# Kernel tuning notes

Hardware: AMD Instinct MI355X
Metric: run time of the kernel (lower is better)

## Reference

```python
import jax, jax.numpy as jnp
import numpy as np

B, T, C = 32, 4096, 256


def setup_inputs() -> dict:
    key = jax.random.key(0)
    ks = jax.random.split(key, 10)
    s = lambda *sh: 0.05
    return {
        "gru_output": jax.random.normal(ks[0], (B, T, C), jnp.float32),
        "intensity_curves": jax.random.uniform(ks[1], (B, T), jnp.float32),
        "W1": jax.random.normal(ks[2], (C, 128), jnp.float32) * 0.05,
        "b1": jnp.zeros((128,), jnp.float32),
        "W2": jax.random.normal(ks[3], (128, 64), jnp.float32) * 0.05,
        "b2": jnp.zeros((64,), jnp.float32),
        "W3": jax.random.normal(ks[4], (64, 4), jnp.float32) * 0.05,
        "b3": jnp.zeros((4,), jnp.float32),
        "conv_w": jax.random.normal(ks[5], (1, C, 3), jnp.float32) * 0.05,  # OIH
        "conv_b": jnp.zeros((1,), jnp.float32),
    }


def reference(gru_output, intensity_curves, W1, b1, W2, b2, W3, b3, conv_w, conv_b):
    Bb, Tt, Cc = gru_output.shape
    # per-timestep phase classifier MLP + softmax -> (B,T,4)
    h = jax.nn.relu(gru_output @ W1 + b1)
    h = jax.nn.relu(h @ W2 + b2)
    phase_probs = jax.nn.softmax(h @ W3 + b3, axis=-1)
    # transition scores: Conv1d(C->1,k=3,pad=1) + sigmoid -> (B,T)
    x = jnp.transpose(gru_output, (0, 2, 1))  # (B,C,T)
    ts = jax.lax.conv_general_dilated(x, conv_w, (1,), 'SAME',
                                      dimension_numbers=('NCH', 'OIH', 'NCH'))
    transition_scores = jax.nn.sigmoid(ts[:, 0, :] + conv_b[0])  # (B,T)
    # run-length segments: new segment when dominant phase changes or transition>0.7
    dom = jnp.argmax(phase_probs, axis=-1)  # (B,T) int
    change = (dom[:, 1:] != dom[:, :-1]) | (transition_scores[:, 1:] > 0.7)
    change = jnp.concatenate([jnp.zeros((Bb, 1), bool), change], axis=1)
    seg = jnp.cumsum(change.astype(jnp.int32), axis=1)  # (B,T) segment id per step
    gseg = (seg + jnp.arange(Bb, dtype=jnp.int32)[:, None] * Tt).reshape(-1)
    nseg = Bb * Tt
    cnt = jax.ops.segment_sum(jnp.ones((nseg,), jnp.float32)[: gseg.shape[0]] * 0 + 1.0,
                              gseg, num_segments=nseg)
    sum_int = jax.ops.segment_sum(intensity_curves.reshape(-1), gseg, num_segments=nseg)
    conf_t = jnp.take_along_axis(phase_probs, dom[..., None], axis=2)[..., 0]  # (B,T)
    sum_conf = jax.ops.segment_sum(conf_t.reshape(-1), gseg, num_segments=nseg)
    denom = jnp.maximum(cnt, 1.0)
    mean_int = (sum_int / denom)[gseg].reshape(Bb, Tt)   # segment-mean intensity per step
    mean_conf = (sum_conf / denom)[gseg].reshape(Bb, Tt)  # segment-mean confidence per step
    return phase_probs, transition_scores, seg, mean_int, mean_conf
```

## Files before the change

### kernel.cpp

```cpp
#include <hip/hip_runtime.h>

#define B_ 32
#define T_ 4096
#define C_ 256
#define R_ (B_*T_)
#define H1_ 128
#define H2_ 64

#define TB 32

#define PROBS_OFF 0
#define TS_OFF  (R_*4)
#define SEG_OFF (TS_OFF + R_)
#define MI_OFF  (SEG_OFF + R_)
#define MC_OFF  (MI_OFF + R_)

#define XS_OFF  0
#define XS_P    260
#define W1S_OFF 8320
#define H1S_OFF 8320
#define H1S_P   132
#define H2S_OFF 0
#define H2S_P   68
#define W3S_OFF 2176
#define W3S_P   68
#define SMEMF   12544

__device__ __forceinline__ void fma4(float4& a, float s, const float4& b) {
  a.x = fmaf(s, b.x, a.x); a.y = fmaf(s, b.y, a.y);
  a.z = fmaf(s, b.z, a.z); a.w = fmaf(s, b.w, a.w);
}

__global__ __launch_bounds__(256, 4) void mlp_conv_kernel(
    const float* __restrict__ X, const float* __restrict__ W1, const float* __restrict__ b1,
    const float* __restrict__ W2, const float* __restrict__ b2,
    const float* __restrict__ W3, const float* __restrict__ b3,
    const float* __restrict__ CW, const float* __restrict__ CB,
    float* __restrict__ out)
{
  __shared__ float sm[SMEMF];
  const int tid  = threadIdx.x;
  const int row0 = blockIdx.x * TB;

  float4 st0 = *(const float4*)&W1[0 * 1024 + tid * 4];
  float4 st1 = *(const float4*)&W1[1 * 1024 + tid * 4];
  float4 st2 = *(const float4*)&W1[2 * 1024 + tid * 4];
  float4 st3 = *(const float4*)&W1[3 * 1024 + tid * 4];

  #pragma unroll
  for (int i2 = 0; i2 < 8; ++i2) {
    int g = tid + 256 * i2;
    int r = g >> 6, m = g & 63;
    float4 v = *(const float4*)&X[(size_t)(row0 + r) * C_ + m * 4];
    *(float4*)&sm[XS_OFF + r * XS_P + m * 4] = v;
  }
  __syncthreads();

  {
    const int l = tid & 63, w = tid >> 6;
    const int rowi = w * 8 + (l & 7);
    const int p = l >> 3;
    const int grow = row0 + rowi;
    const int tb = grow & (T_ - 1);
    float s = 0.f;
    #pragma unroll
    for (int cc = 0; cc < 8; ++cc) {
      const int c = p * 32 + cc * 4;
      float4 x0 = *(const float4*)&sm[XS_OFF + rowi * XS_P + c];
      float4 xm, xp;
      if (tb == 0)             xm = make_float4(0.f, 0.f, 0.f, 0.f);
      else if (rowi >= 1)      xm = *(const float4*)&sm[XS_OFF + (rowi - 1) * XS_P + c];
      else                     xm = *(const float4*)&X[(size_t)(grow - 1) * C_ + c];
      if (tb == T_ - 1)        xp = make_float4(0.f, 0.f, 0.f, 0.f);
      else if (rowi + 1 < TB)  xp = *(const float4*)&sm[XS_OFF + (rowi + 1) * XS_P + c];
      else                     xp = *(const float4*)&X[(size_t)(grow + 1) * C_ + c];
      float4 wa = *(const float4*)&CW[c * 3 + 0];
      float4 wb = *(const float4*)&CW[c * 3 + 4];
      float4 wc = *(const float4*)&CW[c * 3 + 8];
      s += xm.x * wa.x + x0.x * wa.y + xp.x * wa.z;
      s += xm.y * wa.w + x0.y * wb.x + xp.y * wb.y;
      s += xm.z * wb.z + x0.z * wb.w + xp.z * wc.x;
      s += xm.w * wc.y + x0.w * wc.z + xp.w * wc.w;
    }
    s += __shfl_xor(s, 8);
    s += __shfl_xor(s, 16);
    s += __shfl_xor(s, 32);
    if (p == 0) out[TS_OFF + grow] = 1.f / (1.f + expf(-(s + CB[0])));
  }

  const int rt = tid >> 5, ct = tid & 31;
  const int rb = rt * 4;
  float4 acc0 = make_float4(0.f, 0.f, 0.f, 0.f);
  float4 acc1 = acc0, acc2 = acc0, acc3 = acc0;
  for (int kc = 0; kc < 8; ++kc) {
    *(float4*)&sm[W1S_OFF + 0 * 1024 + tid * 4] = st0;
    *(float4*)&sm[W1S_OFF + 1 * 1024 + tid * 4] = st1;
    *(float4*)&sm[W1S_OFF + 2 * 1024 + tid * 4] = st2;
    *(float4*)&sm[W1S_OFF + 3 * 1024 + tid * 4] = st3;
    __syncthreads();
    if (kc + 1 < 8) {
      const float* wp = W1 + (size_t)(kc + 1) * 4096;
      st0 = *(const float4*)&wp[0 * 1024 + tid * 4];
      st1 = *(const float4*)&wp[1 * 1024 + tid * 4];
      st2 = *(const float4*)&wp[2 * 1024 + tid * 4];
      st3 = *(const float4*)&wp[3 * 1024 + tid * 4];
    }
    #pragma unroll
    for (int k4 = 0; k4 < 8; ++k4) {
      const int kb = kc * 32 + k4 * 4;
      float4 a0 = *(const float4*)&sm[XS_OFF + (rb + 0) * XS_P + kb];
      float4 a1 = *(const float4*)&sm[XS_OFF + (rb + 1) * XS_P + kb];
      float4 a2 = *(const float4*)&sm[XS_OFF + (rb + 2) * XS_P + kb];
      float4 a3 = *(const float4*)&sm[XS_OFF + (rb + 3) * XS_P + kb];
      float4 q0 = *(const float4*)&sm[W1S_OFF + (k4 * 4 + 0) * H1_ + ct * 4];
      float4 q1 = *(const float4*)&sm[W1S_OFF + (k4 * 4 + 1) * H1_ + ct * 4];
      float4 q2 = *(const float4*)&sm[W1S_OFF + (k4 * 4 + 2) * H1_ + ct * 4];
      float4 q3 = *(const float4*)&sm[W1S_OFF + (k4 * 4 + 3) * H1_ + ct * 4];
      fma4(acc0, a0.x, q0); fma4(acc0, a0.y, q1); fma4(acc0, a0.z, q2); fma4(acc0, a0.w, q3);
      fma4(acc1, a1.x, q0); fma4(acc1, a1.y, q1); fma4(acc1, a1.z, q2); fma4(acc1, a1.w, q3);
      fma4(acc2, a2.x, q0); fma4(acc2, a2.y, q1); fma4(acc2, a2.z, q2); fma4(acc2, a2.w, q3);
      fma4(acc3, a3.x, q0); fma4(acc3, a3.y, q1); fma4(acc3, a3.z, q2); fma4(acc3, a3.w, q3);
    }
    __syncthreads();
  }

  {
    float4 bb = *(const float4*)&b1[ct * 4];
    float4 h;
    h = acc0; h.x = fmaxf(h.x + bb.x, 0.f); h.y = fmaxf(h.y + bb.y, 0.f);
              h.z = fmaxf(h.z + bb.z, 0.f); h.w = fmaxf(h.w + bb.w, 0.f);
    *(float4*)&sm[H1S_OFF + (rb + 0) * H1S_P + ct * 4] = h;
    h = acc1; h.x = fmaxf(h.x + bb.x, 0.f); h.y = fmaxf(h.y + bb.y, 0.f);
              h.z = fmaxf(h.z + bb.z, 0.f); h.w = fmaxf(h.w + bb.w, 0.f);
    *(float4*)&sm[H1S_OFF + (rb + 1) * H1S_P + ct * 4] = h;
    h = acc2; h.x = fmaxf(h.x + bb.x, 0.f); h.y = fmaxf(h.y + bb.y, 0.f);
              h.z = fmaxf(h.z + bb.z, 0.f); h.w = fmaxf(h.w + bb.w, 0.f);
    *(float4*)&sm[H1S_OFF + (rb + 2) * H1S_P + ct * 4] = h;
    h = acc3; h.x = fmaxf(h.x + bb.x, 0.f); h.y = fmaxf(h.y + bb.y, 0.f);
              h.z = fmaxf(h.z + bb.z, 0.f); h.w = fmaxf(h.w + bb.w, 0.f);
    *(float4*)&sm[H1S_OFF + (rb + 3) * H1S_P + ct * 4] = h;
  }
  __syncthreads();

  {
    const int rt2 = tid >> 4, ct2 = tid & 15;
    const float* w2p = W2 + ct2 * 4;
    float4 Wc0 = *(const float4*)&w2p[0 * H2_];
    float4 Wc1 = *(const float4*)&w2p[1 * H2_];
    float4 Wc2 = *(const float4*)&w2p[2 * H2_];
    float4 Wc3 = *(const float4*)&w2p[3 * H2_];
    float4 c0 = make_float4(0.f, 0.f, 0.f, 0.f), c1 = c0;
    #pragma unroll
    for (int k4 = 0; k4 < 32; ++k4) {
      const int rn = (k4 < 31) ? (k4 + 1) * 4 : k4 * 4;
      float4 Wn0 = *(const float4*)&w2p[(rn + 0) * H2_];
      float4 Wn1 = *(const float4*)&w2p[(rn + 1) * H2_];
      float4 Wn2 = *(const float4*)&w2p[(rn + 2) * H2_];
      float4 Wn3 = *(const float4*)&w2p[(rn + 3) * H2_];
      float4 a0 = *(const float4*)&sm[H1S_OFF + (rt2 * 2 + 0) * H1S_P + k4 * 4];
      float4 a1 = *(const float4*)&sm[H1S_OFF + (rt2 * 2 + 1) * H1S_P + k4 * 4];
      fma4(c0, a0.x, Wc0); fma4(c0, a0.y, Wc1); fma4(c0, a0.z, Wc2); fma4(c0, a0.w, Wc3);
      fma4(c1, a1.x, Wc0); fma4(c1, a1.y, Wc1); fma4(c1, a1.z, Wc2); fma4(c1, a1.w, Wc3);
      Wc0 = Wn0; Wc1 = Wn1; Wc2 = Wn2; Wc3 = Wn3;
    }
    float4 bb = *(const float4*)&b2[ct2 * 4];
    c0.x = fmaxf(c0.x + bb.x, 0.f); c0.y = fmaxf(c0.y + bb.y, 0.f);
    c0.z = fmaxf(c0.z + bb.z, 0.f); c0.w = fmaxf(c0.w + bb.w, 0.f);
    c1.x = fmaxf(c1.x + bb.x, 0.f); c1.y = fmaxf(c1.y + bb.y, 0.f);
    c1.z = fmaxf(c1.z + bb.z, 0.f); c1.w = fmaxf(c1.w + bb.w, 0.f);
    *(float4*)&sm[H2S_OFF + (rt2 * 2 + 0) * H2S_P + ct2 * 4] = c0;
    *(float4*)&sm[H2S_OFF + (rt2 * 2 + 1) * H2S_P + ct2 * 4] = c1;
  }
  {
    int k = tid >> 2, j = tid & 3;
    sm[W3S_OFF + j * W3S_P + k] = W3[tid];
  }
  __syncthreads();

  if (tid < 128) {
    const int row = tid >> 2, j = tid & 3;
    float4 ps = make_float4(0.f, 0.f, 0.f, 0.f);
    #pragma unroll
    for (int k4 = 0; k4 < 16; ++k4) {
      float4 a = *(const float4*)&sm[H2S_OFF + row * H2S_P + k4 * 4];
      float4 w = *(const float4*)&sm[W3S_OFF + j * W3S_P + k4 * 4];
      ps.x = fmaf(a.x, w.x, ps.x);
      ps.y = fmaf(a.y, w.y, ps.y);
      ps.z = fmaf(a.z, w.z, ps.z);
      ps.w = fmaf(a.w, w.w, ps.w);
    }
    float l = ((ps.x + ps.y) + (ps.z + ps.w)) + b3[j];
    float n1v = __shfl_xor(l, 1);
    float n2v = __shfl_xor(l, 2);
    float n3v = __shfl_xor(l, 3);
    float L0 = (j == 0) ? l : (j == 1) ? n1v : (j == 2) ? n2v : n3v;
    float L1 = (j == 1) ? l : (j == 0) ? n1v : (j == 2) ? n3v : n2v;
    float L2 = (j == 2) ? l : (j == 0) ? n2v : (j == 1) ? n3v : n1v;
    float L3 = (j == 3) ? l : (j == 0) ? n3v : (j == 1) ? n2v : n1v;
    float mx = fmaxf(fmaxf(L0, L1), fmaxf(L2, L3));
    float e0 = expf(L0 - mx), e1 = expf(L1 - mx), e2 = expf(L2 - mx), e3 = expf(L3 - mx);
    float inv = 1.f / ((e0 + e1) + (e2 + e3));
    float p0 = e0 * inv, p1 = e1 * inv, p2 = e2 * inv, p3 = e3 * inv;
    const int grow = row0 + row;
    float pown = (j == 0) ? p0 : (j == 1) ? p1 : (j == 2) ? p2 : p3;
    out[PROBS_OFF + (size_t)grow * 4 + j] = pown;
    if (j == 0) {
      int dom = 0; float pm = p0;
      if (p1 > pm) { pm = p1; dom = 1; }
      if (p2 > pm) { pm = p2; dom = 2; }
      if (p3 > pm) { pm = p3; dom = 3; }
      out[MI_OFF + grow] = (float)dom;
      out[MC_OFF + grow] = pm;
    }
  }
}

__global__ __launch_bounds__(1024, 1) void seg_kernel(
    const float* __restrict__ inten, float* __restrict__ out)
{
  __shared__ float scnt[T_], ssi[T_], ssc[T_];
  __shared__ int wtot[16], wexcl[16];
  const int tid = threadIdx.x;
  const int lane = tid & 63, wid = tid >> 6;
  const size_t base = (size_t)blockIdx.x * T_;
  const float* tsS = out + TS_OFF;
  float* segO = out + SEG_OFF;
  float* miO  = out + MI_OFF;
  float* mcO  = out + MC_OFF;
  const int t4 = tid * 4;

  float4 dv = *(const float4*)&miO[base + t4];
  float4 tv = *(const float4*)&tsS[base + t4];
  float4 iv = *(const float4*)&inten[base + t4];
  float4 cv = *(const float4*)&mcO[base + t4];
  float pd = (tid == 0) ? 0.f : miO[base + t4 - 1];

  for (int i = tid; i < T_; i += 1024) { scnt[i] = 0.f; ssi[i] = 0.f; ssc[i] = 0.f; }

  int c0 = (t4 == 0) ? 0 : (((dv.x != pd)   || (tv.x > 0.7f)) ? 1 : 0);
  int c1 = ((dv.y != dv.x) || (tv.y > 0.7f)) ? 1 : 0;
  int c2 = ((dv.z != dv.y) || (tv.z > 0.7f)) ? 1 : 0;
  int c3 = ((dv.w != dv.z) || (tv.w > 0.7f)) ? 1 : 0;
  int l0 = c0, l1 = c0 + c1, l2 = l1 + c2, l3 = l2 + c3;
  const int tsum = l3;

  int v = tsum;
  #pragma unroll
  for (int d = 1; d < 64; d <<= 1) {
    int o = __shfl_up(v, (unsigned)d);
    if (lane >= d) v += o;
  }
  if (lane == 63) wtot[wid] = v;
  __syncthreads();
  if (tid < 16) {
    int x = wtot[tid];
    int xx = x;
    #pragma unroll
    for (int d = 1; d < 16; d <<= 1) {
      int o = __shfl_up(xx, (unsigned)d);
      if (tid >= d) xx += o;
    }
    wexcl[tid] = xx - x;
  }
  __syncthreads();
  const int texcl = wexcl[wid] + (v - tsum);
  const int s0 = texcl + l0, s1 = texcl + l1, s2 = texcl + l2, s3 = texcl + l3;

  {
    int cur = s0; float aI = iv.x, aC = cv.x, aN = 1.f;
    if (s1 == cur) { aI += iv.y; aC += cv.y; aN += 1.f; }
    else { atomicAdd(&ssi[cur], aI); atomicAdd(&ssc[cur], aC); atomicAdd(&scnt[cur], aN);
           cur = s1; aI = iv.y; aC = cv.y; aN = 1.f; }
    if (s2 == cur) { aI += iv.z; aC += cv.z; aN += 1.f; }
    else { atomicAdd(&ssi[cur], aI); atomicAdd(&ssc[cur], aC); atomicAdd(&scnt[cur], aN);
           cur = s2; aI = iv.z; aC = cv.z; aN = 1.f; }
    if (s3 == cur) { aI += iv.w; aC += cv.w; aN += 1.f; }
    else { atomicAdd(&ssi[cur], aI); atomicAdd(&ssc[cur], aC); atomicAdd(&scnt[cur], aN);
           cur = s3; aI = iv.w; aC = cv.w; aN = 1.f; }
    atomicAdd(&ssi[cur], aI); atomicAdd(&ssc[cur], aC); atomicAdd(&scnt[cur], aN);
  }
  __syncthreads();

  float n0 = scnt[s0], n1 = scnt[s1], n2 = scnt[s2], n3 = scnt[s3];
  float4 m4, q4, g4;
  m4.x = ssi[s0] / n0; m4.y = ssi[s1] / n1; m4.z = ssi[s2] / n2; m4.w = ssi[s3] / n3;
  q4.x = ssc[s0] / n0; q4.y = ssc[s1] / n1; q4.z = ssc[s2] / n2; q4.w = ssc[s3] / n3;
  g4.x = (float)s0; g4.y = (float)s1; g4.z = (float)s2; g4.w = (float)s3;
  *(float4*)&segO[base + t4] = g4;
  *(float4*)&miO[base + t4]  = m4;
  *(float4*)&mcO[base + t4]  = q4;
}

extern "C" void kernel_launch(void* const* d_in, const int* in_sizes, int n_in,
                              void* d_out, int out_size, void* d_ws, size_t ws_size,
                              hipStream_t stream) {
  (void)in_sizes; (void)n_in; (void)out_size; (void)d_ws; (void)ws_size;
  const float* X   = (const float*)d_in[0];
  const float* INT = (const float*)d_in[1];
  const float* W1  = (const float*)d_in[2];
  const float* B1  = (const float*)d_in[3];
  const float* W2  = (const float*)d_in[4];
  const float* B2  = (const float*)d_in[5];
  const float* W3  = (const float*)d_in[6];
  const float* B3  = (const float*)d_in[7];
  const float* CW  = (const float*)d_in[8];
  const float* CB  = (const float*)d_in[9];
  float* out = (float*)d_out;

  hipLaunchKernelGGL(mlp_conv_kernel, dim3(R_ / TB), dim3(256), 0, stream,
                     X, W1, B1, W2, B2, W3, B3, CW, CB, out);
  hipLaunchKernelGGL(seg_kernel, dim3(B_), dim3(1024), 0, stream, INT, out);
}
```

Measured before the change: 205.8 us.

## Stage W2 in shared memory, prefetch it during layer 1, fuse layer 3 via shuffles

W2 is now prefetched into registers during the last layer-1 iteration and stored to shared memory, so layer 2 reads weights from LDS instead of per-thread global loads. Layer 3 and the softmax are computed directly from the layer-2 register results with a cross-lane shuffle reduction, which removes the H2 shared-memory staging and one barrier. Probabilities are written as one float4 per row. This raises register pressure from the extra prefetched W2/W3 values, which may affect occupancy.

```diff
diff --git a/kernel.cpp b/kernel.cpp
--- a/kernel.cpp
+++ b/kernel.cpp
@@ -20,10 +20,7 @@
 #define W1S_OFF 8320
 #define H1S_OFF 8320
 #define H1S_P   132
-#define H2S_OFF 0
-#define H2S_P   68
-#define W3S_OFF 2176
-#define W3S_P   68
+#define W2S_OFF 0
 #define SMEMF   12544
 
 __device__ __forceinline__ void fma4(float4& a, float s, const float4& b) {
@@ -104,6 +101,11 @@
       st1 = *(const float4*)&wp[1 * 1024 + tid * 4];
       st2 = *(const float4*)&wp[2 * 1024 + tid * 4];
       st3 = *(const float4*)&wp[3 * 1024 + tid * 4];
+    } else {
+      st0 = ((const float4*)W2)[tid +   0];
+      st1 = ((const float4*)W2)[tid + 256];
+      st2 = ((const float4*)W2)[tid + 512];
+      st3 = ((const float4*)W2)[tid + 768];
     }
     #pragma unroll
     for (int k4 = 0; k4 < 8; ++k4) {
@@ -124,6 +126,16 @@
     __syncthreads();
   }
 
+  const int ct2 = tid & 15;
+  float4 t4a = ((const float4*)W2)[tid + 1024];
+  float4 t4b = ((const float4*)W2)[tid + 1280];
+  float4 t4c = ((const float4*)W2)[tid + 1536];
+  float4 t4d = ((const float4*)W2)[tid + 1792];
+  float4 w30 = ((const float4*)W3)[ct2 * 4 + 0];
+  float4 w31 = ((const float4*)W3)[ct2 * 4 + 1];
+  float4 w32 = ((const float4*)W3)[ct2 * 4 + 2];
+  float4 w33 = ((const float4*)W3)[ct2 * 4 + 3];
+  float4 b3v = *(const float4*)&b3[0];
   {
     float4 bb = *(const float4*)&b1[ct * 4];
     float4 h;
@@ -140,71 +152,57 @@
               h.z = fmaxf(h.z + bb.z, 0.f); h.w = fmaxf(h.w + bb.w, 0.f);
     *(float4*)&sm[H1S_OFF + (rb + 3) * H1S_P + ct * 4] = h;
   }
-  __syncthreads();
-
-  {
-    const int rt2 = tid >> 4, ct2 = tid & 15;
-    const float* w2p = W2 + ct2 * 4;
-    float4 Wc0 = *(const float4*)&w2p[0 * H2_];
-    float4 Wc1 = *(const float4*)&w2p[1 * H2_];
-    float4 Wc2 = *(const float4*)&w2p[2 * H2_];
-    float4 Wc3 = *(const float4*)&w2p[3 * H2_];
-    float4 c0 = make_float4(0.f, 0.f, 0.f, 0.f), c1 = c0;
-    #pragma unroll
-    for (int k4 = 0; k4 < 32; ++k4) {
-      const int rn = (k4 < 31) ? (k4 + 1) * 4 : k4 * 4;
-      float4 Wn0 = *(const float4*)&w2p[(rn + 0) * H2_];
-      float4 Wn1 = *(const float4*)&w2p[(rn + 1) * H2_];
-      float4 Wn2 = *(const float4*)&w2p[(rn + 2) * H2_];
-      float4 Wn3 = *(const float4*)&w2p[(rn + 3) * H2_];
-      float4 a0 = *(const float4*)&sm[H1S_OFF + (rt2 * 2 + 0) * H1S_P + k4 * 4];
-      float4 a1 = *(const float4*)&sm[H1S_OFF + (rt2 * 2 + 1) * H1S_P + k4 * 4];
-      fma4(c0, a0.x, Wc0); fma4(c0, a0.y, Wc1); fma4(c0, a0.z, Wc2); fma4(c0, a0.w, Wc3);
-      fma4(c1, a1.x, Wc0); fma4(c1, a1.y, Wc1); fma4(c1, a1.z, Wc2); fma4(c1, a1.w, Wc3);
-      Wc0 = Wn0; Wc1 = Wn1; Wc2 = Wn2; Wc3 = Wn3;
-    }
+  *(float4*)&sm[W2S_OFF + (tid +    0) * 4] = st0;
+  *(float4*)&sm[W2S_OFF + (tid +  256) * 4] = st1;
+  *(float4*)&sm[W2S_OFF + (tid +  512) * 4] = st2;
+  *(float4*)&sm[W2S_OFF + (tid +  768) * 4] = st3;
+  *(float4*)&sm[W2S_OFF + (tid + 1024) * 4] = t4a;
+  *(float4*)&sm[W2S_OFF + (tid + 1280) * 4] = t4b;
+  *(float4*)&sm[W2S_OFF + (tid + 1536) * 4] = t4c;
+  *(float4*)&sm[W2S_OFF + (tid + 1792) * 4] = t4d;
+  __syncthreads();
+
+  const int rt2 = tid >> 4;
+  float4 c0 = make_float4(0.f, 0.f, 0.f, 0.f), c1 = c0;
+  #pragma unroll 8
+  for (int k4 = 0; k4 < 32; ++k4) {
+    float4 a0 = *(const float4*)&sm[H1S_OFF + (rt2 * 2 + 0) * H1S_P + k4 * 4];
+    float4 a1 = *(const float4*)&sm[H1S_OFF + (rt2 * 2 + 1) * H1S_P + k4 * 4];
+    float4 q0 = *(const float4*)&sm[W2S_OFF + (k4 * 4 + 0) * H2_ + ct2 * 4];
+    float4 q1 = *(const float4*)&sm[W2S_OFF + (k4 * 4 + 1) * H2_ + ct2 * 4];
+    float4 q2 = *(const float4*)&sm[W2S_OFF + (k4 * 4 + 2) * H2_ + ct2 * 4];
+    float4 q3 = *(const float4*)&sm[W2S_OFF + (k4 * 4 + 3) * H2_ + ct2 * 4];
+    fma4(c0, a0.x, q0); fma4(c0, a0.y, q1); fma4(c0, a0.z, q2); fma4(c0, a0.w, q3);
+    fma4(c1, a1.x, q0); fma4(c1, a1.y, q1); fma4(c1, a1.z, q2); fma4(c1, a1.w, q3);
+  }
+  {
     float4 bb = *(const float4*)&b2[ct2 * 4];
     c0.x = fmaxf(c0.x + bb.x, 0.f); c0.y = fmaxf(c0.y + bb.y, 0.f);
     c0.z = fmaxf(c0.z + bb.z, 0.f); c0.w = fmaxf(c0.w + bb.w, 0.f);
     c1.x = fmaxf(c1.x + bb.x, 0.f); c1.y = fmaxf(c1.y + bb.y, 0.f);
     c1.z = fmaxf(c1.z + bb.z, 0.f); c1.w = fmaxf(c1.w + bb.w, 0.f);
-    *(float4*)&sm[H2S_OFF + (rt2 * 2 + 0) * H2S_P + ct2 * 4] = c0;
-    *(float4*)&sm[H2S_OFF + (rt2 * 2 + 1) * H2S_P + ct2 * 4] = c1;
-  }
-  {
-    int k = tid >> 2, j = tid & 3;
-    sm[W3S_OFF + j * W3S_P + k] = W3[tid];
-  }
-  __syncthreads();
-
-  if (tid < 128) {
-    const int row = tid >> 2, j = tid & 3;
-    float4 ps = make_float4(0.f, 0.f, 0.f, 0.f);
-    #pragma unroll
-    for (int k4 = 0; k4 < 16; ++k4) {
-      float4 a = *(const float4*)&sm[H2S_OFF + row * H2S_P + k4 * 4];
-      float4 w = *(const float4*)&sm[W3S_OFF + j * W3S_P + k4 * 4];
-      ps.x = fmaf(a.x, w.x, ps.x);
-      ps.y = fmaf(a.y, w.y, ps.y);
-      ps.z = fmaf(a.z, w.z, ps.z);
-      ps.w = fmaf(a.w, w.w, ps.w);
-    }
-    float l = ((ps.x + ps.y) + (ps.z + ps.w)) + b3[j];
-    float n1v = __shfl_xor(l, 1);
-    float n2v = __shfl_xor(l, 2);
-    float n3v = __shfl_xor(l, 3);
-    float L0 = (j == 0) ? l : (j == 1) ? n1v : (j == 2) ? n2v : n3v;
-    float L1 = (j == 1) ? l : (j == 0) ? n1v : (j == 2) ? n3v : n2v;
-    float L2 = (j == 2) ? l : (j == 0) ? n2v : (j == 1) ? n3v : n1v;
-    float L3 = (j == 3) ? l : (j == 0) ? n3v : (j == 1) ? n2v : n1v;
-    float mx = fmaxf(fmaxf(L0, L1), fmaxf(L2, L3));
-    float e0 = expf(L0 - mx), e1 = expf(L1 - mx), e2 = expf(L2 - mx), e3 = expf(L3 - mx);
+  }
+
+  float4 L0 = make_float4(0.f, 0.f, 0.f, 0.f), L1 = L0;
+  fma4(L0, c0.x, w30); fma4(L0, c0.y, w31); fma4(L0, c0.z, w32); fma4(L0, c0.w, w33);
+  fma4(L1, c1.x, w30); fma4(L1, c1.y, w31); fma4(L1, c1.z, w32); fma4(L1, c1.w, w33);
+  #pragma unroll
+  for (int d = 1; d < 16; d <<= 1) {
+    L0.x += __shfl_xor(L0.x, d); L0.y += __shfl_xor(L0.y, d);
+    L0.z += __shfl_xor(L0.z, d); L0.w += __shfl_xor(L0.w, d);
+    L1.x += __shfl_xor(L1.x, d); L1.y += __shfl_xor(L1.y, d);
+    L1.z += __shfl_xor(L1.z, d); L1.w += __shfl_xor(L1.w, d);
+  }
+  {
+    float4 L = (ct2 < 8) ? L0 : L1;
+    const int grow = row0 + rt2 * 2 + ((ct2 < 8) ? 0 : 1);
+    L.x += b3v.x; L.y += b3v.y; L.z += b3v.z; L.w += b3v.w;
+    float mx = fmaxf(fmaxf(L.x, L.y), fmaxf(L.z, L.w));
+    float e0 = expf(L.x - mx), e1 = expf(L.y - mx), e2 = expf(L.z - mx), e3 = expf(L.w - mx);
     float inv = 1.f / ((e0 + e1) + (e2 + e3));
     float p0 = e0 * inv, p1 = e1 * inv, p2 = e2 * inv, p3 = e3 * inv;
-    const int grow = row0 + row;
-    float pown = (j == 0) ? p0 : (j == 1) ? p1 : (j == 2) ? p2 : p3;
-    out[PROBS_OFF + (size_t)grow * 4 + j] = pown;
-    if (j == 0) {
+    if ((ct2 & 7) == 0) {
+      *(float4*)&out[PROBS_OFF + (size_t)grow * 4] = make_float4(p0, p1, p2, p3);
       int dom = 0; float pm = p0;
       if (p1 > pm) { pm = p1; dom = 1; }
       if (p2 > pm) { pm = p2; dom = 2; }
```

New measurement: 206.5 us. Within noise of the previous version (+0.3%).

## Restructure MLP layers to use scalar-loaded operands broadcast across wave lanes

Applied to the files above, without the earlier changes.

Layer 1 now gives each wave 8 rows, reads the X rows through scalar s_load instructions (wave-uniform) and takes W1 columns from LDS, so each lane computes 2 output columns. Layer 2 splits the 64 outputs across waves and streams W2 rows via s_load_dwordx16, with each lane owning one row. Layer 3 uses scalar-loaded W3 and reduces partial logits through LDS. The aim is to cut LDS traffic and vector register use by using the scalar memory path. The cost is serialized s_waitcnt stalls on scalar loads, and the scalar load of X skips the LDS copy already staged in shared memory.

```diff
diff --git a/kernel.cpp b/kernel.cpp
--- a/kernel.cpp
+++ b/kernel.cpp
@@ -17,19 +17,15 @@
 
 #define XS_OFF  0
 #define XS_P    260
-#define W1S_OFF 8320
-#define H1S_OFF 8320
-#define H1S_P   132
-#define H2S_OFF 0
-#define H2S_P   68
-#define W3S_OFF 2176
-#define W3S_P   68
-#define SMEMF   12544
-
-__device__ __forceinline__ void fma4(float4& a, float s, const float4& b) {
-  a.x = fmaf(s, b.x, a.x); a.y = fmaf(s, b.y, a.y);
-  a.z = fmaf(s, b.z, a.z); a.w = fmaf(s, b.w, a.w);
-}
+#define W1S_OFF 0
+#define H1S_OFF 4096
+#define H1S_P   130
+#define LG_OFF  0
+#define LG_P    17
+#define SMEMF   8320
+
+typedef float f4s  __attribute__((ext_vector_type(4)));
+typedef float f16s __attribute__((ext_vector_type(16)));
 
 __global__ __launch_bounds__(256, 4) void mlp_conv_kernel(
     const float* __restrict__ X, const float* __restrict__ W1, const float* __restrict__ b1,
@@ -40,12 +36,14 @@
 {
   __shared__ float sm[SMEMF];
   const int tid  = threadIdx.x;
+  const int l    = tid & 63;
+  const int w    = tid >> 6;
   const int row0 = blockIdx.x * TB;
 
-  float4 st0 = *(const float4*)&W1[0 * 1024 + tid * 4];
-  float4 st1 = *(const float4*)&W1[1 * 1024 + tid * 4];
-  float4 st2 = *(const float4*)&W1[2 * 1024 + tid * 4];
-  float4 st3 = *(const float4*)&W1[3 * 1024 + tid * 4];
+  float4 st0 = *(const float4*)&W1[(tid +   0) * 4];
+  float4 st1 = *(const float4*)&W1[(tid + 256) * 4];
+  float4 st2 = *(const float4*)&W1[(tid + 512) * 4];
+  float4 st3 = *(const float4*)&W1[(tid + 768) * 4];
 
   #pragma unroll
   for (int i2 = 0; i2 < 8; ++i2) {
@@ -57,7 +55,6 @@
   __syncthreads();
 
   {
-    const int l = tid & 63, w = tid >> 6;
     const int rowi = w * 8 + (l & 7);
     const int p = l >> 3;
     const int grow = row0 + rowi;
@@ -87,116 +84,155 @@
     s += __shfl_xor(s, 32);
     if (p == 0) out[TS_OFF + grow] = 1.f / (1.f + expf(-(s + CB[0])));
   }
-
-  const int rt = tid >> 5, ct = tid & 31;
-  const int rb = rt * 4;
-  float4 acc0 = make_float4(0.f, 0.f, 0.f, 0.f);
-  float4 acc1 = acc0, acc2 = acc0, acc3 = acc0;
+  __syncthreads();
+
+  const int wvu = __builtin_amdgcn_readfirstlane(w);
+  const float* xw = X + (size_t)(row0 + wvu * 8) * C_;
+  float2 acc[8];
+  #pragma unroll
+  for (int r = 0; r < 8; ++r) acc[r] = make_float2(0.f, 0.f);
+
   for (int kc = 0; kc < 8; ++kc) {
-    *(float4*)&sm[W1S_OFF + 0 * 1024 + tid * 4] = st0;
-    *(float4*)&sm[W1S_OFF + 1 * 1024 + tid * 4] = st1;
-    *(float4*)&sm[W1S_OFF + 2 * 1024 + tid * 4] = st2;
-    *(float4*)&sm[W1S_OFF + 3 * 1024 + tid * 4] = st3;
+    *(float4*)&sm[W1S_OFF + (tid +   0) * 4] = st0;
+    *(float4*)&sm[W1S_OFF + (tid + 256) * 4] = st1;
+    *(float4*)&sm[W1S_OFF + (tid + 512) * 4] = st2;
+    *(float4*)&sm[W1S_OFF + (tid + 768) * 4] = st3;
     __syncthreads();
     if (kc + 1 < 8) {
       const float* wp = W1 + (size_t)(kc + 1) * 4096;
-      st0 = *(const float4*)&wp[0 * 1024 + tid * 4];
-      st1 = *(const float4*)&wp[1 * 1024 + tid * 4];
-      st2 = *(const float4*)&wp[2 * 1024 + tid * 4];
-      st3 = *(const float4*)&wp[3 * 1024 + tid * 4];
-    }
-    #pragma unroll
-    for (int k4 = 0; k4 < 8; ++k4) {
-      const int kb = kc * 32 + k4 * 4;
-      float4 a0 = *(const float4*)&sm[XS_OFF + (rb + 0) * XS_P + kb];
-      float4 a1 = *(const float4*)&sm[XS_OFF + (rb + 1) * XS_P + kb];
-      float4 a2 = *(const float4*)&sm[XS_OFF + (rb + 2) * XS_P + kb];
-      float4 a3 = *(const float4*)&sm[XS_OFF + (rb + 3) * XS_P + kb];
-      float4 q0 = *(const float4*)&sm[W1S_OFF + (k4 * 4 + 0) * H1_ + ct * 4];
-      float4 q1 = *(const float4*)&sm[W1S_OFF + (k4 * 4 + 1) * H1_ + ct * 4];
-      float4 q2 = *(const float4*)&sm[W1S_OFF + (k4 * 4 + 2) * H1_ + ct * 4];
-      float4 q3 = *(const float4*)&sm[W1S_OFF + (k4 * 4 + 3) * H1_ + ct * 4];
-      fma4(acc0, a0.x, q0); fma4(acc0, a0.y, q1); fma4(acc0, a0.z, q2); fma4(acc0, a0.w, q3);
-      fma4(acc1, a1.x, q0); fma4(acc1, a1.y, q1); fma4(acc1, a1.z, q2); fma4(acc1, a1.w, q3);
-      fma4(acc2, a2.x, q0); fma4(acc2, a2.y, q1); fma4(acc2, a2.z, q2); fma4(acc2, a2.w, q3);
-      fma4(acc3, a3.x, q0); fma4(acc3, a3.y, q1); fma4(acc3, a3.z, q2); fma4(acc3, a3.w, q3);
+      st0 = *(const float4*)&wp[(tid +   0) * 4];
+      st1 = *(const float4*)&wp[(tid + 256) * 4];
+      st2 = *(const float4*)&wp[(tid + 512) * 4];
+      st3 = *(const float4*)&wp[(tid + 768) * 4];
+    }
+    #pragma unroll
+    for (int ka = 0; ka < 8; ++ka) {
+      const float* xka = xw + kc * 32 + ka * 4;
+      f4s a0, a1, a2, a3, a4, a5, a6, a7;
+      asm volatile(
+        "s_load_dwordx4 %0, %8, 0x0\n\t"
+        "s_load_dwordx4 %1, %8, 0x400\n\t"
+        "s_load_dwordx4 %2, %8, 0x800\n\t"
+        "s_load_dwordx4 %3, %8, 0xc00\n\t"
+        "s_load_dwordx4 %4, %8, 0x1000\n\t"
+        "s_load_dwordx4 %5, %8, 0x1400\n\t"
+        "s_load_dwordx4 %6, %8, 0x1800\n\t"
+        "s_load_dwordx4 %7, %8, 0x1c00\n\t"
+        "s_waitcnt lgkmcnt(0)"
+        : "=&s"(a0), "=&s"(a1), "=&s"(a2), "=&s"(a3),
+          "=&s"(a4), "=&s"(a5), "=&s"(a6), "=&s"(a7)
+        : "s"(xka));
+      #pragma unroll
+      for (int kk = 0; kk < 4; ++kk) {
+        const int krow = ka * 4 + kk;
+        float2 bv = *(const float2*)&sm[W1S_OFF + krow * H1_ + 2 * l];
+        #define G1R(r, av) { float as_ = (av)[kk]; \
+          acc[r].x = fmaf(as_, bv.x, acc[r].x); \
+          acc[r].y = fmaf(as_, bv.y, acc[r].y); }
+        G1R(0, a0) G1R(1, a1) G1R(2, a2) G1R(3, a3)
+        G1R(4, a4) G1R(5, a5) G1R(6, a6) G1R(7, a7)
+        #undef G1R
+      }
     }
     __syncthreads();
   }
 
   {
-    float4 bb = *(const float4*)&b1[ct * 4];
-    float4 h;
-    h = acc0; h.x = fmaxf(h.x + bb.x, 0.f); h.y = fmaxf(h.y + bb.y, 0.f);
-              h.z = fmaxf(h.z + bb.z, 0.f); h.w = fmaxf(h.w + bb.w, 0.f);
-    *(float4*)&sm[H1S_OFF + (rb + 0) * H1S_P + ct * 4] = h;
-    h = acc1; h.x = fmaxf(h.x + bb.x, 0.f); h.y = fmaxf(h.y + bb.y, 0.f);
-              h.z = fmaxf(h.z + bb.z, 0.f); h.w = fmaxf(h.w + bb.w, 0.f);
-    *(float4*)&sm[H1S_OFF + (rb + 1) * H1S_P + ct * 4] = h;
-    h = acc2; h.x = fmaxf(h.x + bb.x, 0.f); h.y = fmaxf(h.y + bb.y, 0.f);
-              h.z = fmaxf(h.z + bb.z, 0.f); h.w = fmaxf(h.w + bb.w, 0.f);
-    *(float4*)&sm[H1S_OFF + (rb + 2) * H1S_P + ct * 4] = h;
-    h = acc3; h.x = fmaxf(h.x + bb.x, 0.f); h.y = fmaxf(h.y + bb.y, 0.f);
-              h.z = fmaxf(h.z + bb.z, 0.f); h.w = fmaxf(h.w + bb.w, 0.f);
-    *(float4*)&sm[H1S_OFF + (rb + 3) * H1S_P + ct * 4] = h;
-  }
-  __syncthreads();
-
-  {
-    const int rt2 = tid >> 4, ct2 = tid & 15;
-    const float* w2p = W2 + ct2 * 4;
-    float4 Wc0 = *(const float4*)&w2p[0 * H2_];
-    float4 Wc1 = *(const float4*)&w2p[1 * H2_];
-    float4 Wc2 = *(const float4*)&w2p[2 * H2_];
-    float4 Wc3 = *(const float4*)&w2p[3 * H2_];
-    float4 c0 = make_float4(0.f, 0.f, 0.f, 0.f), c1 = c0;
-    #pragma unroll
-    for (int k4 = 0; k4 < 32; ++k4) {
-      const int rn = (k4 < 31) ? (k4 + 1) * 4 : k4 * 4;
-      float4 Wn0 = *(const float4*)&w2p[(rn + 0) * H2_];
-      float4 Wn1 = *(const float4*)&w2p[(rn + 1) * H2_];
-      float4 Wn2 = *(const float4*)&w2p[(rn + 2) * H2_];
-      float4 Wn3 = *(const float4*)&w2p[(rn + 3) * H2_];
-      float4 a0 = *(const float4*)&sm[H1S_OFF + (rt2 * 2 + 0) * H1S_P + k4 * 4];
-      float4 a1 = *(const float4*)&sm[H1S_OFF + (rt2 * 2 + 1) * H1S_P + k4 * 4];
-      fma4(c0, a0.x, Wc0); fma4(c0, a0.y, Wc1); fma4(c0, a0.z, Wc2); fma4(c0, a0.w, Wc3);
-      fma4(c1, a1.x, Wc0); fma4(c1, a1.y, Wc1); fma4(c1, a1.z, Wc2); fma4(c1, a1.w, Wc3);
-      Wc0 = Wn0; Wc1 = Wn1; Wc2 = Wn2; Wc3 = Wn3;
-    }
-    float4 bb = *(const float4*)&b2[ct2 * 4];
-    c0.x = fmaxf(c0.x + bb.x, 0.f); c0.y = fmaxf(c0.y + bb.y, 0.f);
-    c0.z = fmaxf(c0.z + bb.z, 0.f); c0.w = fmaxf(c0.w + bb.w, 0.f);
-    c1.x = fmaxf(c1.x + bb.x, 0.f); c1.y = fmaxf(c1.y + bb.y, 0.f);
-    c1.z = fmaxf(c1.z + bb.z, 0.f); c1.w = fmaxf(c1.w + bb.w, 0.f);
-    *(float4*)&sm[H2S_OFF + (rt2 * 2 + 0) * H2S_P + ct2 * 4] = c0;
-    *(float4*)&sm[H2S_OFF + (rt2 * 2 + 1) * H2S_P + ct2 * 4] = c1;
-  }
-  {
-    int k = tid >> 2, j = tid & 3;
-    sm[W3S_OFF + j * W3S_P + k] = W3[tid];
+    float2 b1v = *(const float2*)&b1[2 * l];
+    #pragma unroll
+    for (int r = 0; r < 8; ++r) {
+      float2 h;
+      h.x = fmaxf(acc[r].x + b1v.x, 0.f);
+      h.y = fmaxf(acc[r].y + b1v.y, 0.f);
+      *(float2*)&sm[H1S_OFF + (wvu * 8 + r) * H1S_P + 2 * l] = h;
+    }
+  }
+  __syncthreads();
+
+  const int rr = l & 31;
+  const int abase = H1S_OFF + rr * H1S_P;
+  const float* w2w = W2 + wvu * 16;
+  float4 acc2[4];
+  #pragma unroll
+  for (int j = 0; j < 4; ++j) acc2[j] = make_float4(0.f, 0.f, 0.f, 0.f);
+  for (int g = 0; g < 64; ++g) {
+    const float* w2k = w2w + (size_t)g * 128;
+    f16s B0, B1;
+    asm volatile(
+      "s_load_dwordx16 %0, %2, 0x0\n\t"
+      "s_load_dwordx16 %1, %2, 0x100\n\t"
+      "s_waitcnt lgkmcnt(0)"
+      : "=&s"(B0), "=&s"(B1)
+      : "s"(w2k));
+    float2 av = *(const float2*)&sm[abase + 2 * g];
+    #define G2K(av_, Bv) { float a_ = (av_); \
+      acc2[0].x = fmaf(a_, (Bv)[0],  acc2[0].x); acc2[0].y = fmaf(a_, (Bv)[1],  acc2[0].y); \
+      acc2[0].z = fmaf(a_, (Bv)[2],  acc2[0].z); acc2[0].w = fmaf(a_, (Bv)[3],  acc2[0].w); \
+      acc2[1].x = fmaf(a_, (Bv)[4],  acc2[1].x); acc2[1].y = fmaf(a_, (Bv)[5],  acc2[1].y); \
+      acc2[1].z = fmaf(a_, (Bv)[6],  acc2[1].z); acc2[1].w = fmaf(a_, (Bv)[7],  acc2[1].w); \
+      acc2[2].x = fmaf(a_, (Bv)[8],  acc2[2].x); acc2[2].y = fmaf(a_, (Bv)[9],  acc2[2].y); \
+      acc2[2].z = fmaf(a_, (Bv)[10], acc2[2].z); acc2[2].w = fmaf(a_, (Bv)[11], acc2[2].w); \
+      acc2[3].x = fmaf(a_, (Bv)[12], acc2[3].x); acc2[3].y = fmaf(a_, (Bv)[13], acc2[3].y); \
+      acc2[3].z = fmaf(a_, (Bv)[14], acc2[3].z); acc2[3].w = fmaf(a_, (Bv)[15], acc2[3].w); }
+    G2K(av.x, B0)
+    G2K(av.y, B1)
+    #undef G2K
+  }
+
+  float h2[16];
+  {
+    const float* b2w = b2 + wvu * 16;
+    #pragma unroll
+    for (int j = 0; j < 4; ++j) {
+      h2[j*4+0] = fmaxf(((const float*)&acc2[j])[0] + b2w[j*4+0], 0.f);
+      h2[j*4+1] = fmaxf(((const float*)&acc2[j])[1] + b2w[j*4+1], 0.f);
+      h2[j*4+2] = fmaxf(((const float*)&acc2[j])[2] + b2w[j*4+2], 0.f);
+      h2[j*4+3] = fmaxf(((const float*)&acc2[j])[3] + b2w[j*4+3], 0.f);
+    }
+  }
+  float4 L = make_float4(0.f, 0.f, 0.f, 0.f);
+  {
+    const float* w3w = W3 + wvu * 64;
+    f16s C0, C1, C2, C3;
+    asm volatile(
+      "s_load_dwordx16 %0, %2, 0x0\n\t"
+      "s_load_dwordx16 %1, %2, 0x40\n\t"
+      "s_waitcnt lgkmcnt(0)"
+      : "=&s"(C0), "=&s"(C1) : "s"(w3w));
+    asm volatile(
+      "s_load_dwordx16 %0, %2, 0x80\n\t"
+      "s_load_dwordx16 %1, %2, 0xc0\n\t"
+      "s_waitcnt lgkmcnt(0)"
+      : "=&s"(C2), "=&s"(C3) : "s"(w3w));
+    #define G3C(c, Cv) { float hh = h2[c]; \
+      L.x = fmaf(hh, (Cv)[((c)&3)*4+0], L.x); L.y = fmaf(hh, (Cv)[((c)&3)*4+1], L.y); \
+      L.z = fmaf(hh, (Cv)[((c)&3)*4+2], L.z); L.w = fmaf(hh, (Cv)[((c)&3)*4+3], L.w); }
+    G3C(0,C0)  G3C(1,C0)  G3C(2,C0)  G3C(3,C0)
+    G3C(4,C1)  G3C(5,C1)  G3C(6,C1)  G3C(7,C1)
+    G3C(8,C2)  G3C(9,C2)  G3C(10,C2) G3C(11,C2)
+    G3C(12,C3) G3C(13,C3) G3C(14,C3) G3C(15,C3)
+    #undef G3C
+  }
+  if (l < 32) {
+    sm[LG_OFF + rr * LG_P + wvu * 4 + 0] = L.x;
+    sm[LG_OFF + rr * LG_P + wvu * 4 + 1] = L.y;
+    sm[LG_OFF + rr * LG_P + wvu * 4 + 2] = L.z;
+    sm[LG_OFF + rr * LG_P + wvu * 4 + 3] = L.w;
   }
   __syncthreads();
 
   if (tid < 128) {
     const int row = tid >> 2, j = tid & 3;
-    float4 ps = make_float4(0.f, 0.f, 0.f, 0.f);
-    #pragma unroll
-    for (int k4 = 0; k4 < 16; ++k4) {
-      float4 a = *(const float4*)&sm[H2S_OFF + row * H2S_P + k4 * 4];
-      float4 w = *(const float4*)&sm[W3S_OFF + j * W3S_P + k4 * 4];
-      ps.x = fmaf(a.x, w.x, ps.x);
-      ps.y = fmaf(a.y, w.y, ps.y);
-      ps.z = fmaf(a.z, w.z, ps.z);
-      ps.w = fmaf(a.w, w.w, ps.w);
-    }
-    float l = ((ps.x + ps.y) + (ps.z + ps.w)) + b3[j];
-    float n1v = __shfl_xor(l, 1);
-    float n2v = __shfl_xor(l, 2);
-    float n3v = __shfl_xor(l, 3);
-    float L0 = (j == 0) ? l : (j == 1) ? n1v : (j == 2) ? n2v : n3v;
-    float L1 = (j == 1) ? l : (j == 0) ? n1v : (j == 2) ? n3v : n2v;
-    float L2 = (j == 2) ? l : (j == 0) ? n2v : (j == 1) ? n3v : n1v;
-    float L3 = (j == 3) ? l : (j == 0) ? n3v : (j == 1) ? n2v : n1v;
+    float lsum = (sm[LG_OFF + row * LG_P + 0 + j] + sm[LG_OFF + row * LG_P + 4 + j])
+               + (sm[LG_OFF + row * LG_P + 8 + j] + sm[LG_OFF + row * LG_P + 12 + j]);
+    float lv = lsum + b3[j];
+    float n1v = __shfl_xor(lv, 1);
+    float n2v = __shfl_xor(lv, 2);
+    float n3v = __shfl_xor(lv, 3);
+    float L0 = (j == 0) ? lv : (j == 1) ? n1v : (j == 2) ? n2v : n3v;
+    float L1 = (j == 1) ? lv : (j == 0) ? n1v : (j == 2) ? n3v : n2v;
+    float L2 = (j == 2) ? lv : (j == 0) ? n2v : (j == 1) ? n3v : n1v;
+    float L3 = (j == 3) ? lv : (j == 0) ? n3v : (j == 1) ? n2v : n1v;
     float mx = fmaxf(fmaxf(L0, L1), fmaxf(L2, L3));
     float e0 = expf(L0 - mx), e1 = expf(L1 - mx), e2 = expf(L2 - mx), e3 = expf(L3 - mx);
     float inv = 1.f / ((e0 + e1) + (e2 + e3));
```

Result: slower. 308.2 us (+49.8%).
